# Kernel tuning notes

Measured on AMD Instinct MI355X. Metric: run time of the kernel, lower is better.

The kernel has to match this reference:

```python
import jax, jax.numpy as jnp
import numpy as np


def setup_inputs() -> dict:
    key = jax.random.key(0)
    k1, k2, k3 = jax.random.split(key, 3)
    B, C, L, D = 2, 8, 256, 128
    start_hidden = jax.random.normal(k1, (B, C, L, D), dtype=jnp.float32)
    end_hidden = jax.random.normal(k2, (B, C, L, D), dtype=jnp.float32)
    # nn.Parameter initialized uniform_(-0.1, 0.1)
    v = jax.random.uniform(k3, (D,), dtype=jnp.float32, minval=-0.1, maxval=0.1)
    return {"start_hidden": start_hidden, "end_hidden": end_hidden, "v": v}


def reference(start_hidden, end_hidden, v):
    # start_hidden: [B, C, L, D], end_hidden: [B, C, L, D], v: [D]
    # additive pairwise scoring: tanh(s_i + e_j) . v  for every (i, j) span
    add_hidden = jnp.tanh(start_hidden[:, :, :, None, :] + end_hidden[:, :, None, :, :])  # [B,C,L,L,D]
    res = jnp.einsum('bcnmd,d->bcnm', add_hidden, v)  # [B, C, L, L]
    span_ner_mat_tensor = jnp.transpose(res, (0, 2, 3, 1))  # [B, L, L, C]
    return span_ner_mat_tensor
```

## Files before the change

kernel.cpp:

```cpp
#include <hip/hip_runtime.h>


#define LDIM 256
#define DDIM 128
#define DPAD 132

__global__ __launch_bounds__(256) void span_tanh_dot_kernel(
    const float* __restrict__ start_h,
    const float* __restrict__ end_h,
    const float* __restrict__ v,
    float* __restrict__ out,
    int C)
{
    __shared__ float s_t[32][DPAD];
    __shared__ float e_t[32][DPAD];
    __shared__ float s_vsum;

    const int bc = blockIdx.z;
    const int i0 = blockIdx.y * 32;
    const int j0 = blockIdx.x * 32;
    const int tx = threadIdx.x;
    const int ty = threadIdx.y;
    const int tid = ty * 16 + tx;

    const float K = 2.8853900817779268f;

    const float* sg = start_h + ((size_t)bc * LDIM + i0) * DDIM;
    const float* eg = end_h   + ((size_t)bc * LDIM + j0) * DDIM;

    #pragma unroll
    for (int k = 0; k < 4; ++k) {
        const int idx = tid + k * 256;
        const int r  = idx >> 5;
        const int c4 = (idx & 31) << 2;
        float4 a = *(const float4*)(sg + r * DDIM + c4);
        a.x = __builtin_amdgcn_exp2f(K * a.x);
        a.y = __builtin_amdgcn_exp2f(K * a.y);
        a.z = __builtin_amdgcn_exp2f(K * a.z);
        a.w = __builtin_amdgcn_exp2f(K * a.w);
        *(float4*)(&s_t[r][c4]) = a;
        float4 b = *(const float4*)(eg + r * DDIM + c4);
        b.x = __builtin_amdgcn_exp2f(K * b.x);
        b.y = __builtin_amdgcn_exp2f(K * b.y);
        b.z = __builtin_amdgcn_exp2f(K * b.z);
        b.w = __builtin_amdgcn_exp2f(K * b.w);
        *(float4*)(&e_t[r][c4]) = b;
    }

    if (tid < 64) {
        float2 vv = *(const float2*)(v + 2 * tid);
        float p = vv.x + vv.y;
        #pragma unroll
        for (int off = 32; off > 0; off >>= 1) p += __shfl_down(p, off);
        if (tid == 0) s_vsum = p;
    }
    __syncthreads();

    float acc00 = 0.f, acc01 = 0.f, acc10 = 0.f, acc11 = 0.f;

#define QUAD(ACC, S, E)                                            \
    {                                                              \
        float q0 = fmaf((S).x, (E).x, 1.0f);                       \
        float q1 = fmaf((S).y, (E).y, 1.0f);                       \
        float q2 = fmaf((S).z, (E).z, 1.0f);                       \
        float q3 = fmaf((S).w, (E).w, 1.0f);                       \
        float ab = q0 * q1, cd = q2 * q3;                          \
        float n01 = fmaf(v0, q1, v1 * q0);                         \
        float n23 = fmaf(v2, q3, v3 * q2);                         \
        float N = fmaf(n01, cd, n23 * ab);                         \
        float r = __builtin_amdgcn_rcpf(ab * cd);                  \
        ACC = fmaf(N, r, ACC);                                     \
    }

    #pragma unroll 4
    for (int d = 0; d < DDIM; d += 4) {
        const float4 sa = *(const float4*)(&s_t[ty     ][d]);
        const float4 sb = *(const float4*)(&s_t[ty + 16][d]);
        const float4 ea = *(const float4*)(&e_t[tx     ][d]);
        const float4 eb = *(const float4*)(&e_t[tx + 16][d]);
        const float v0 = v[d], v1 = v[d + 1], v2 = v[d + 2], v3 = v[d + 3];

        QUAD(acc00, sa, ea);
        QUAD(acc01, sa, eb);
        QUAD(acc10, sb, ea);
        QUAD(acc11, sb, eb);
    }
#undef QUAD

    const int b_ = bc / C;
    const int c_ = bc - b_ * C;
    const float Sv = s_vsum;
    const int ia = i0 + ty, ib = i0 + ty + 16;
    const int ja = j0 + tx, jb = j0 + tx + 16;
    const size_t base = ((size_t)b_ * LDIM) * LDIM * C + c_;

    out[base + ((size_t)ia * LDIM + ja) * C] = fmaf(-2.f, acc00, Sv);
    out[base + ((size_t)ia * LDIM + jb) * C] = fmaf(-2.f, acc01, Sv);
    out[base + ((size_t)ib * LDIM + ja) * C] = fmaf(-2.f, acc10, Sv);
    out[base + ((size_t)ib * LDIM + jb) * C] = fmaf(-2.f, acc11, Sv);
}

extern "C" void kernel_launch(void* const* d_in, const int* in_sizes, int n_in,
                              void* d_out, int out_size, void* d_ws, size_t ws_size,
                              hipStream_t stream) {
    const float* start_h = (const float*)d_in[0];
    const float* end_h   = (const float*)d_in[1];
    const float* v       = (const float*)d_in[2];
    float* out = (float*)d_out;

    const int BC = in_sizes[0] / (LDIM * DDIM);
    const int C  = 8;

    dim3 grid(LDIM / 32, LDIM / 32, BC);
    dim3 block(16, 16);
    span_tanh_dot_kernel<<<grid, block, 0, stream>>>(start_h, end_h, v, out, C);
}
```

Before: 19.68 us.

## Split D reduction across two thread halves with 512-thread blocks

Doubles the block to 512 threads arranged as 8x8x8. Each 32x32 tile is now covered by four 16x16 quadrants times two halves of the D dimension, and each thread accumulates over 64 d values instead of 128. The two partial sums are combined through a shared-memory float4 buffer before the output is written. The aim is more waves and more latency hiding per block, at the cost of an extra barrier, extra LDS traffic, and half the threads sitting idle during the final stores.

```diff
diff --git a/kernel.cpp b/kernel.cpp
--- a/kernel.cpp
+++ b/kernel.cpp
@@ -5,7 +5,7 @@
 #define DDIM 128
 #define DPAD 132
 
-__global__ __launch_bounds__(256) void span_tanh_dot_kernel(
+__global__ __launch_bounds__(512, 8) void span_tanh_dot_kernel(
     const float* __restrict__ start_h,
     const float* __restrict__ end_h,
     const float* __restrict__ v,
@@ -14,6 +14,7 @@
 {
     __shared__ float s_t[32][DPAD];
     __shared__ float e_t[32][DPAD];
+    __shared__ float4 red[4 * 64];
     __shared__ float s_vsum;
 
     const int bc = blockIdx.z;
@@ -21,7 +22,13 @@
     const int j0 = blockIdx.x * 32;
     const int tx = threadIdx.x;
     const int ty = threadIdx.y;
-    const int tid = ty * 16 + tx;
+    const int g  = threadIdx.z;
+    const int t  = ty * 8 + tx;
+    const int tid = g * 64 + t;
+
+    const int q  = g & 3;
+    const int h  = g >> 2;
+    const int qi = q >> 1, qj = q & 1;
 
     const float K = 2.8853900817779268f;
 
@@ -29,8 +36,8 @@
     const float* eg = end_h   + ((size_t)bc * LDIM + j0) * DDIM;
 
     #pragma unroll
-    for (int k = 0; k < 4; ++k) {
-        const int idx = tid + k * 256;
+    for (int k = 0; k < 2; ++k) {
+        const int idx = tid + k * 512;
         const int r  = idx >> 5;
         const int c4 = (idx & 31) << 2;
         float4 a = *(const float4*)(sg + r * DDIM + c4);
@@ -47,14 +54,18 @@
         *(float4*)(&e_t[r][c4]) = b;
     }
 
-    if (tid < 64) {
-        float2 vv = *(const float2*)(v + 2 * tid);
+    if (g == 0) {
+        float2 vv = *(const float2*)(v + 2 * t);
         float p = vv.x + vv.y;
         #pragma unroll
-        for (int off = 32; off > 0; off >>= 1) p += __shfl_down(p, off);
-        if (tid == 0) s_vsum = p;
+        for (int off = 1; off < 64; off <<= 1) p += __shfl_xor(p, off);
+        if (t == 0) s_vsum = p;
     }
     __syncthreads();
+
+    const int r0 = qi * 16 + ty;
+    const int c0 = qj * 16 + tx;
+    const int dbase = __builtin_amdgcn_readfirstlane(h * 64);
 
     float acc00 = 0.f, acc01 = 0.f, acc10 = 0.f, acc11 = 0.f;
 
@@ -72,12 +83,13 @@
         ACC = fmaf(N, r, ACC);                                     \
     }
 
-    #pragma unroll 4
-    for (int d = 0; d < DDIM; d += 4) {
-        const float4 sa = *(const float4*)(&s_t[ty     ][d]);
-        const float4 sb = *(const float4*)(&s_t[ty + 16][d]);
-        const float4 ea = *(const float4*)(&e_t[tx     ][d]);
-        const float4 eb = *(const float4*)(&e_t[tx + 16][d]);
+    #pragma unroll 2
+    for (int it = 0; it < 16; ++it) {
+        const int d = dbase + it * 4;
+        const float4 sa = *(const float4*)(&s_t[r0    ][d]);
+        const float4 sb = *(const float4*)(&s_t[r0 + 8][d]);
+        const float4 ea = *(const float4*)(&e_t[c0    ][d]);
+        const float4 eb = *(const float4*)(&e_t[c0 + 8][d]);
         const float v0 = v[d], v1 = v[d + 1], v2 = v[d + 2], v3 = v[d + 3];
 
         QUAD(acc00, sa, ea);
@@ -87,17 +99,24 @@
     }
 #undef QUAD
 
-    const int b_ = bc / C;
-    const int c_ = bc - b_ * C;
-    const float Sv = s_vsum;
-    const int ia = i0 + ty, ib = i0 + ty + 16;
-    const int ja = j0 + tx, jb = j0 + tx + 16;
-    const size_t base = ((size_t)b_ * LDIM) * LDIM * C + c_;
+    if (h == 1) red[q * 64 + t] = make_float4(acc00, acc01, acc10, acc11);
+    __syncthreads();
+    if (h == 0) {
+        const float4 p = red[q * 64 + t];
+        acc00 += p.x; acc01 += p.y; acc10 += p.z; acc11 += p.w;
 
-    out[base + ((size_t)ia * LDIM + ja) * C] = fmaf(-2.f, acc00, Sv);
-    out[base + ((size_t)ia * LDIM + jb) * C] = fmaf(-2.f, acc01, Sv);
-    out[base + ((size_t)ib * LDIM + ja) * C] = fmaf(-2.f, acc10, Sv);
-    out[base + ((size_t)ib * LDIM + jb) * C] = fmaf(-2.f, acc11, Sv);
+        const int b_ = bc / C;
+        const int c_ = bc - b_ * C;
+        const float Sv = s_vsum;
+        const int ia = i0 + r0, ib = ia + 8;
+        const int ja = j0 + c0, jb = ja + 8;
+        const size_t basea = (((size_t)b_ * LDIM + ia) * LDIM) * C + c_;
+        const size_t baseb = (((size_t)b_ * LDIM + ib) * LDIM) * C + c_;
+        out[basea + (size_t)ja * C] = fmaf(-2.f, acc00, Sv);
+        out[basea + (size_t)jb * C] = fmaf(-2.f, acc01, Sv);
+        out[baseb + (size_t)ja * C] = fmaf(-2.f, acc10, Sv);
+        out[baseb + (size_t)jb * C] = fmaf(-2.f, acc11, Sv);
+    }
 }
 
 extern "C" void kernel_launch(void* const* d_in, const int* in_sizes, int n_in,
@@ -112,6 +131,6 @@
     const int C  = 8;
 
     dim3 grid(LDIM / 32, LDIM / 32, BC);
-    dim3 block(16, 16);
+    dim3 block(8, 8, 8);
     span_tanh_dot_kernel<<<grid, block, 0, stream>>>(start_h, end_h, v, out, C);
 }
```

Result: no change. 19.55 us (-0.7%).

## Split D across wavefront groups with 4x4 register tiles and LDS reduction

Applied to the files above, without the earlier changes.

The 256-thread block becomes 8x8x4. Each of the four groups handles a 32-wide slice of D and computes a 4x4 output micro-tile per thread, so each LDS float4 load feeds more QUAD operations. Partial sums are parked in the reused start-tile LDS buffer and summed across groups before the strided output store. This adds an extra barrier, LDS traffic for the reduction and more registers per thread, in exchange for fewer LDS reads per unit of math.

```diff
diff --git a/kernel.cpp b/kernel.cpp
--- a/kernel.cpp
+++ b/kernel.cpp
@@ -12,16 +12,19 @@
     float* __restrict__ out,
     int C)
 {
-    __shared__ float s_t[32][DPAD];
+    __shared__ float s_pool[32 * DPAD];
     __shared__ float e_t[32][DPAD];
     __shared__ float s_vsum;
+    float (*s_t)[DPAD] = (float (*)[DPAD])s_pool;
 
     const int bc = blockIdx.z;
     const int i0 = blockIdx.y * 32;
     const int j0 = blockIdx.x * 32;
     const int tx = threadIdx.x;
     const int ty = threadIdx.y;
-    const int tid = ty * 16 + tx;
+    const int g  = threadIdx.z;
+    const int t  = ty * 8 + tx;
+    const int tid = g * 64 + t;
 
     const float K = 2.8853900817779268f;
 
@@ -47,16 +50,21 @@
         *(float4*)(&e_t[r][c4]) = b;
     }
 
-    if (tid < 64) {
-        float2 vv = *(const float2*)(v + 2 * tid);
+    if (g == 0) {
+        float2 vv = *(const float2*)(v + 2 * t);
         float p = vv.x + vv.y;
         #pragma unroll
-        for (int off = 32; off > 0; off >>= 1) p += __shfl_down(p, off);
-        if (tid == 0) s_vsum = p;
+        for (int off = 1; off < 64; off <<= 1) p += __shfl_xor(p, off);
+        if (t == 0) s_vsum = p;
     }
     __syncthreads();
 
-    float acc00 = 0.f, acc01 = 0.f, acc10 = 0.f, acc11 = 0.f;
+    const int dbase = __builtin_amdgcn_readfirstlane(g) * 32;
+
+    float acc00 = 0.f, acc01 = 0.f, acc02 = 0.f, acc03 = 0.f;
+    float acc10 = 0.f, acc11 = 0.f, acc12 = 0.f, acc13 = 0.f;
+    float acc20 = 0.f, acc21 = 0.f, acc22 = 0.f, acc23 = 0.f;
+    float acc30 = 0.f, acc31 = 0.f, acc32 = 0.f, acc33 = 0.f;
 
 #define QUAD(ACC, S, E)                                            \
     {                                                              \
@@ -72,32 +80,56 @@
         ACC = fmaf(N, r, ACC);                                     \
     }
 
-    #pragma unroll 4
-    for (int d = 0; d < DDIM; d += 4) {
-        const float4 sa = *(const float4*)(&s_t[ty     ][d]);
-        const float4 sb = *(const float4*)(&s_t[ty + 16][d]);
-        const float4 ea = *(const float4*)(&e_t[tx     ][d]);
-        const float4 eb = *(const float4*)(&e_t[tx + 16][d]);
+    #pragma unroll 2
+    for (int it = 0; it < 8; ++it) {
+        const int d = dbase + it * 4;
+        const float4 s0 = *(const float4*)(&s_t[ty     ][d]);
+        const float4 s1 = *(const float4*)(&s_t[ty +  8][d]);
+        const float4 s2 = *(const float4*)(&s_t[ty + 16][d]);
+        const float4 s3 = *(const float4*)(&s_t[ty + 24][d]);
+        const float4 e0 = *(const float4*)(&e_t[tx     ][d]);
+        const float4 e1 = *(const float4*)(&e_t[tx +  8][d]);
+        const float4 e2 = *(const float4*)(&e_t[tx + 16][d]);
+        const float4 e3 = *(const float4*)(&e_t[tx + 24][d]);
         const float v0 = v[d], v1 = v[d + 1], v2 = v[d + 2], v3 = v[d + 3];
 
-        QUAD(acc00, sa, ea);
-        QUAD(acc01, sa, eb);
-        QUAD(acc10, sb, ea);
-        QUAD(acc11, sb, eb);
+        QUAD(acc00, s0, e0); QUAD(acc01, s0, e1); QUAD(acc02, s0, e2); QUAD(acc03, s0, e3);
+        QUAD(acc10, s1, e0); QUAD(acc11, s1, e1); QUAD(acc12, s1, e2); QUAD(acc13, s1, e3);
+        QUAD(acc20, s2, e0); QUAD(acc21, s2, e1); QUAD(acc22, s2, e2); QUAD(acc23, s2, e3);
+        QUAD(acc30, s3, e0); QUAD(acc31, s3, e1); QUAD(acc32, s3, e2); QUAD(acc33, s3, e3);
     }
 #undef QUAD
+
+    __syncthreads();
+    float* red = s_pool;
+#define PARK(A, B, ACC) red[(((A) * 4 + (B)) * 4 + g) * 64 + t] = ACC;
+    PARK(0,0,acc00) PARK(0,1,acc01) PARK(0,2,acc02) PARK(0,3,acc03)
+    PARK(1,0,acc10) PARK(1,1,acc11) PARK(1,2,acc12) PARK(1,3,acc13)
+    PARK(2,0,acc20) PARK(2,1,acc21) PARK(2,2,acc22) PARK(2,3,acc23)
+    PARK(3,0,acc30) PARK(3,1,acc31) PARK(3,2,acc32) PARK(3,3,acc33)
+#undef PARK
+    __syncthreads();
+
+#define COMB(B)                                                    \
+    (red[((g * 4 + (B)) * 4 + 0) * 64 + t] +                       \
+     red[((g * 4 + (B)) * 4 + 1) * 64 + t] +                       \
+     red[((g * 4 + (B)) * 4 + 2) * 64 + t] +                       \
+     red[((g * 4 + (B)) * 4 + 3) * 64 + t])
+    const float o0 = COMB(0);
+    const float o1 = COMB(1);
+    const float o2 = COMB(2);
+    const float o3 = COMB(3);
+#undef COMB
 
     const int b_ = bc / C;
     const int c_ = bc - b_ * C;
     const float Sv = s_vsum;
-    const int ia = i0 + ty, ib = i0 + ty + 16;
-    const int ja = j0 + tx, jb = j0 + tx + 16;
-    const size_t base = ((size_t)b_ * LDIM) * LDIM * C + c_;
-
-    out[base + ((size_t)ia * LDIM + ja) * C] = fmaf(-2.f, acc00, Sv);
-    out[base + ((size_t)ia * LDIM + jb) * C] = fmaf(-2.f, acc01, Sv);
-    out[base + ((size_t)ib * LDIM + ja) * C] = fmaf(-2.f, acc10, Sv);
-    out[base + ((size_t)ib * LDIM + jb) * C] = fmaf(-2.f, acc11, Sv);
+    const int i = i0 + ty + 8 * g;
+    const size_t rowbase = (((size_t)b_ * LDIM + i) * LDIM) * C + c_;
+    out[rowbase + (size_t)(j0 + tx     ) * C] = fmaf(-2.f, o0, Sv);
+    out[rowbase + (size_t)(j0 + tx +  8) * C] = fmaf(-2.f, o1, Sv);
+    out[rowbase + (size_t)(j0 + tx + 16) * C] = fmaf(-2.f, o2, Sv);
+    out[rowbase + (size_t)(j0 + tx + 24) * C] = fmaf(-2.f, o3, Sv);
 }
 
 extern "C" void kernel_launch(void* const* d_in, const int* in_sizes, int n_in,
@@ -112,6 +144,6 @@
     const int C  = 8;
 
     dim3 grid(LDIM / 32, LDIM / 32, BC);
-    dim3 block(16, 16);
+    dim3 block(8, 8, 4);
     span_tanh_dot_kernel<<<grid, block, 0, stream>>>(start_h, end_h, v, out, C);
 }
```

Result: faster. 19.04 us (-3.3%).
